# Performance work log

Measured on AMD Instinct MI355X. Metric: run time of the kernel, lower is better.

Reference implementation:

```python
import jax, jax.numpy as jnp
import numpy as np

# ---- hash-grid constants (from tcnn Encoding config in __init__) ----
N_LEVELS = 16
F = 2                      # n_features_per_level
LOG2_T = 19
T = 1 << LOG2_T            # hashmap entries per level
BASE_RES = 16
PER_LEVEL_SCALE = 1.447269237440378
PRIMES = np.array([1, 2654435761, 805459861], dtype=np.uint32)
# corner offsets of the unit cube, shape [8, 3]
OFFS = np.stack(np.meshgrid([0, 1], [0, 1], [0, 1], indexing='ij'), -1).reshape(8, 3)


def hash_grid_encode(x01, table):
    """x01: [N,3] in [0,1]; table: [L, T, F]. Returns [N, L*F]."""
    offs = jnp.asarray(OFFS, dtype=jnp.int32)          # [8,3]
    primes = jnp.asarray(PRIMES)                       # [3] uint32
    feats = []
    for l in range(N_LEVELS):
        scale = BASE_RES * (PER_LEVEL_SCALE ** l) - 1.0   # tcnn grid scale
        res = int(np.ceil(scale)) + 1                      # grid resolution
        pos = x01 * scale + 0.5                            # [N,3]
        pos0 = jnp.floor(pos)
        w = pos - pos0                                     # trilinear fracs [N,3]
        pos0 = pos0.astype(jnp.int32)
        corners = jnp.clip(pos0[:, None, :] + offs[None], 0, res - 1)  # [N,8,3]
        if res ** 3 <= T:
            # dense (stride) indexing fits in the table
            idx = (corners[..., 0]
                   + res * corners[..., 1]
                   + res * res * corners[..., 2]).astype(jnp.int32)    # [N,8]
        else:
            # spatial hash with uint32 wraparound multiply + xor
            cu = corners.astype(jnp.uint32)
            idx = ((cu[..., 0] * primes[0])
                   ^ (cu[..., 1] * primes[1])
                   ^ (cu[..., 2] * primes[2])) & jnp.uint32(T - 1)
            idx = idx.astype(jnp.int32)
        # trilinear weights: prod over dims of (w if offset==1 else 1-w)
        wc = jnp.where(offs[None].astype(bool), w[:, None, :], 1.0 - w[:, None, :])
        wc = wc.prod(-1)                                   # [N,8]
        g = table[l][idx]                                  # gather -> [N,8,F]
        feats.append(jnp.einsum('nc,ncf->nf', wc, g))      # [N,F]
    return jnp.concatenate(feats, -1)                      # [N, L*F]


def mlp2(x, w1, w2):
    # 2-layer bias-free MLP with ReLU, matching MLP(num_layers=2, bias=False)
    return jnp.maximum(x @ w1, 0.0) @ w2


def setup_inputs() -> dict:
    key = jax.random.key(0)
    ks = jax.random.split(key, 6)
    N = 1048576
    points = jax.random.uniform(ks[0], (N, 3), jnp.float32, -1.0, 1.0)  # in bbox [-1,1]^3
    # tcnn hash-grid init: uniform(-1e-4, 1e-4)
    hash_table = jax.random.uniform(ks[1], (N_LEVELS, T, F), jnp.float32, -1e-4, 1e-4)
    enc_dim = N_LEVELS * F  # 32
    dw1 = jax.random.normal(ks[2], (enc_dim, 64), jnp.float32) * (1.0 / np.sqrt(enc_dim))
    dw2 = jax.random.normal(ks[3], (64, 1), jnp.float32) * (1.0 / 8.0)
    fw1 = jax.random.normal(ks[4], (enc_dim, 64), jnp.float32) * (1.0 / np.sqrt(enc_dim))
    fw2 = jax.random.normal(ks[5], (64, 3), jnp.float32) * (1.0 / 8.0)
    return {"points": points, "hash_table": hash_table,
            "dw1": dw1, "dw2": dw2, "fw1": fw1, "fw2": fw2}


def reference(points, hash_table, dw1, dw2, fw1, fw2):
    # contract_to_unisphere with bbox [[-1,-1,-1],[1,1,1]] -> [0,1]^3, clamped
    x01 = jnp.clip((points + 1.0) * 0.5, 0.0, 1.0)
    enc = hash_grid_encode(x01, hash_table)               # [N, 32]
    density = jax.nn.softplus(mlp2(enc, dw1, dw2))        # [N, 1]
    color = jax.nn.sigmoid(mlp2(enc, fw1, fw2))           # [N, 3]
    return color, density
```

## Files before the change

### kernel.cpp

```cpp
#include <hip/hip_runtime.h>
#include <hip/hip_bf16.h>
#include <cmath>

#define NLV 16
#define TBL_SIZE (1u << 19)

struct LevelConsts {
    float scale[NLV];
    int   res[NLV];
    int   dense[NLV];
};

__device__ __forceinline__ unsigned int f32_to_bf16_rne(float f) {
    unsigned int u = __float_as_uint(f);
    return (u + 0x7FFFu + ((u >> 16) & 1u)) >> 16;
}
__device__ __forceinline__ unsigned int pack_bf16(float a, float b) {
    return f32_to_bf16_rne(a) | (f32_to_bf16_rne(b) << 16);
}
__device__ __forceinline__ short f32_to_bf16_s(float f) {
    return (short)f32_to_bf16_rne(f);
}
__device__ __forceinline__ float bf16lo_to_f32(unsigned int g) {
    return __uint_as_float(g << 16);
}
__device__ __forceinline__ float bf16hi_to_f32(unsigned int g) {
    return __uint_as_float(g & 0xFFFF0000u);
}

typedef __attribute__((ext_vector_type(8))) short bf16x8;
typedef __attribute__((ext_vector_type(4))) float f32x4;
typedef __attribute__((ext_vector_type(2))) unsigned int u32x2;
typedef __attribute__((ext_vector_type(4))) unsigned int u32x4;

__global__ __launch_bounds__(256) void cvt_table(const float* __restrict__ in,
                                                 unsigned int* __restrict__ out, int npairs) {
    int n2 = npairs >> 1;
    int i = blockIdx.x * 256 + threadIdx.x;
    int stride = gridDim.x * 256;
    const f32x4* in4 = (const f32x4*)in;
    u32x2* out2 = (u32x2*)out;
    for (; i < n2; i += stride) {
        f32x4 v = __builtin_nontemporal_load(&in4[i]);
        u32x2 o;
        o.x = pack_bf16(v.x, v.y);
        o.y = pack_bf16(v.z, v.w);
        __builtin_nontemporal_store(o, &out2[i]);
    }
}

#define ENC_P 4
__global__ __launch_bounds__(256) void encode_lvl(
    const float* __restrict__ points,
    const unsigned int* __restrict__ tbl,
    unsigned int* __restrict__ enc,
    int N, LevelConsts C)
{
    const int level = blockIdx.y;
    const float sc    = C.scale[level];
    const int   res   = C.res[level];
    const int   dense = C.dense[level];
    const unsigned int* __restrict__ t = tbl + (size_t)level * TBL_SIZE;
    unsigned int* __restrict__ eo = enc + (size_t)level * N;

    const int base = blockIdx.x * (256 * ENC_P) + threadIdx.x;

    int   pt[ENC_P];
    int   valid[ENC_P];
    float wx[ENC_P], wy[ENC_P], wz[ENC_P];
    unsigned int i0a[ENC_P][4], i1a[ENC_P][4];

#pragma unroll
    for (int q = 0; q < ENC_P; q++) {
        pt[q] = base + q * 256;
        valid[q] = pt[q] < N;
        int p = valid[q] ? pt[q] : 0;
        float px = __builtin_nontemporal_load(&points[p * 3 + 0]);
        float py = __builtin_nontemporal_load(&points[p * 3 + 1]);
        float pz = __builtin_nontemporal_load(&points[p * 3 + 2]);
        float x = fminf(fmaxf((px + 1.0f) * 0.5f, 0.0f), 1.0f);
        float y = fminf(fmaxf((py + 1.0f) * 0.5f, 0.0f), 1.0f);
        float z = fminf(fmaxf((pz + 1.0f) * 0.5f, 0.0f), 1.0f);

        float fx = x * sc + 0.5f;
        float fy = y * sc + 0.5f;
        float fz = z * sc + 0.5f;
        float f0x = floorf(fx), f0y = floorf(fy), f0z = floorf(fz);
        wx[q] = fx - f0x; wy[q] = fy - f0y; wz[q] = fz - f0z;
        int ix0 = min(max((int)f0x, 0), res - 1);
        int iy0 = min(max((int)f0y, 0), res - 1);
        int iz0 = min(max((int)f0z, 0), res - 1);
        int ix1 = min(ix0 + 1, res - 1);
        int iy1 = min(iy0 + 1, res - 1);
        int iz1 = min(iz0 + 1, res - 1);

#pragma unroll
        for (int m = 0; m < 4; m++) {
            unsigned int uy = (unsigned int)((m & 1) ? iy1 : iy0);
            unsigned int uz = (unsigned int)((m & 2) ? iz1 : iz0);
            unsigned int i0, i1;
            if (dense) {
                unsigned int b = (unsigned int)res * uy + (unsigned int)(res * res) * uz;
                i0 = (unsigned int)ix0 + b;
                i1 = (unsigned int)ix1 + b;
            } else {
                unsigned int H = uy * 2654435761u ^ uz * 805459861u;
                i0 = ((unsigned int)ix0 ^ H) & (TBL_SIZE - 1u);
                i1 = ((unsigned int)ix1 ^ H) & (TBL_SIZE - 1u);
            }
            i0a[q][m] = i0;
            i1a[q][m] = i1;
        }
    }

    u32x2       pr[ENC_P][4];
    unsigned int ex[ENC_P][4];
#pragma unroll
    for (int q = 0; q < ENC_P; q++) {
#pragma unroll
        for (int m = 0; m < 4; m++) {
            unsigned int i0 = i0a[q][m], i1 = i1a[q][m];
            pr[q][m] = *(const u32x2*)(t + (i0 & ~1u));
            unsigned int eidx = (i1 == (i0 ^ 1u)) ? i0 : i1;
            ex[q][m] = t[eidx];
        }
    }

#pragma unroll
    for (int q = 0; q < ENC_P; q++) {
        float e0 = 0.0f, e1 = 0.0f;
        float wxq = wx[q];
#pragma unroll
        for (int m = 0; m < 4; m++) {
            unsigned int i0 = i0a[q][m], i1 = i1a[q][m];
            u32x2 P = pr[q][m];
            unsigned int v0   = (i0 & 1u) ? P.y : P.x;
            unsigned int vpar = (i0 & 1u) ? P.x : P.y;
            unsigned int v1   = (i1 == (i0 ^ 1u)) ? vpar : ex[q][m];
            float wyz = (((m & 1) ? wy[q] : 1.0f - wy[q])) *
                        (((m & 2) ? wz[q] : 1.0f - wz[q]));
            float w0 = wyz * (1.0f - wxq);
            float w1 = wyz * wxq;
            e0 = fmaf(w0, bf16lo_to_f32(v0), e0);
            e0 = fmaf(w1, bf16lo_to_f32(v1), e0);
            e1 = fmaf(w0, bf16hi_to_f32(v0), e1);
            e1 = fmaf(w1, bf16hi_to_f32(v1), e1);
        }
        if (valid[q]) __builtin_nontemporal_store(pack_bf16(e0, e1), &eo[pt[q]]);
    }
}

__global__ __launch_bounds__(256, 4) void mlp_kernel(
    const unsigned int* __restrict__ enc,
    const float* __restrict__ dw1, const float* __restrict__ dw2,
    const float* __restrict__ fw1, const float* __restrict__ fw2,
    float* __restrict__ out, int N, int ntiles)
{
    __shared__ unsigned int hsh[4][16][68];
    __shared__ float sOut[4][256];

    const int tid  = threadIdx.x;
    const int wave = tid >> 6;
    const int lane = tid & 63;
    const int l15 = lane & 15;
    const int quad = lane >> 4;

    bf16x8 B1[8];
#pragma unroll
    for (int nt = 0; nt < 8; nt++) {
        int col = nt * 16 + l15;
        const float* w = (col < 64) ? (dw1 + col) : (fw1 + (col - 64));
#pragma unroll
        for (int j = 0; j < 8; j++) {
            int k = quad * 8 + j;
            B1[nt][j] = f32_to_bf16_s(w[k * 64]);
        }
    }

    bf16x8 B2[4];
#pragma unroll
    for (int s = 0; s < 4; s++) {
#pragma unroll
        for (int j = 0; j < 8; j++) {
            int k_lds = s * 32 + quad * 8 + j;
            int hu = ((k_lds & 7) << 4) | (k_lds >> 3);
            float v = 0.0f;
            if (l15 == 0)      v = (hu < 64)  ? dw2[hu] : 0.0f;
            else if (l15 < 4)  v = (hu >= 64) ? fw2[(hu - 64) * 3 + (l15 - 1)] : 0.0f;
            B2[s][j] = f32_to_bf16_s(v);
        }
    }

    for (int tile = blockIdx.x; tile < ntiles; tile += gridDim.x) {
        const int wbase = tile * 256 + wave * 64;

        unsigned int au[4][4];
#pragma unroll
        for (int sub = 0; sub < 4; sub++) {
            int ptc = min(wbase + sub * 16 + l15, N - 1);
#pragma unroll
            for (int j = 0; j < 4; j++)
                au[sub][j] = enc[(size_t)(quad * 4 + j) * N + ptc];
        }

#pragma unroll
        for (int sub = 0; sub < 4; sub++) {
            union { unsigned int u[4]; bf16x8 v; } acvt;
#pragma unroll
            for (int j = 0; j < 4; j++) acvt.u[j] = au[sub][j];

            f32x4 acc1[8];
#pragma unroll
            for (int nt = 0; nt < 8; nt++) {
                acc1[nt] = (f32x4){0.0f, 0.0f, 0.0f, 0.0f};
                acc1[nt] = __builtin_amdgcn_mfma_f32_16x16x32_bf16(acvt.v, B1[nt], acc1[nt], 0, 0, 0);
            }

#pragma unroll
            for (int r = 0; r < 4; r++) {
                u32x4 pk;
#pragma unroll
                for (int d = 0; d < 4; d++) {
                    float h0 = fmaxf(acc1[2 * d + 0][r], 0.0f);
                    float h1 = fmaxf(acc1[2 * d + 1][r], 0.0f);
                    pk[d] = pack_bf16(h0, h1);
                }
                *(u32x4*)&hsh[wave][quad * 4 + r][l15 * 4] = pk;
            }

            f32x4 p0 = (f32x4){0,0,0,0}, p1 = (f32x4){0,0,0,0};
            f32x4 p2 = (f32x4){0,0,0,0}, p3 = (f32x4){0,0,0,0};
            {
                bf16x8 a0 = *(const bf16x8*)&hsh[wave][l15][0 * 16 + quad * 4];
                bf16x8 a1 = *(const bf16x8*)&hsh[wave][l15][1 * 16 + quad * 4];
                bf16x8 a2 = *(const bf16x8*)&hsh[wave][l15][2 * 16 + quad * 4];
                bf16x8 a3 = *(const bf16x8*)&hsh[wave][l15][3 * 16 + quad * 4];
                p0 = __builtin_amdgcn_mfma_f32_16x16x32_bf16(a0, B2[0], p0, 0, 0, 0);
                p1 = __builtin_amdgcn_mfma_f32_16x16x32_bf16(a1, B2[1], p1, 0, 0, 0);
                p2 = __builtin_amdgcn_mfma_f32_16x16x32_bf16(a2, B2[2], p2, 0, 0, 0);
                p3 = __builtin_amdgcn_mfma_f32_16x16x32_bf16(a3, B2[3], p3, 0, 0, 0);
            }
            f32x4 acc2;
#pragma unroll
            for (int r = 0; r < 4; r++) acc2[r] = (p0[r] + p1[r]) + (p2[r] + p3[r]);

            if (l15 < 4) {
#pragma unroll
                for (int r = 0; r < 4; r++)
                    sOut[wave][(sub * 16 + quad * 4 + r) * 4 + l15] = acc2[r];
            }
        }

        long long cmax = ((long long)N - wbase) * 3;
#pragma unroll
        for (int round = 0; round < 3; round++) {
            int f = round * 64 + lane;
            int lp = f / 3, c = f - lp * 3;
            float v = sOut[wave][lp * 4 + 1 + c];
            v = 1.0f / (1.0f + expf(-v));
            if (f < cmax) out[(size_t)wbase * 3 + f] = v;
        }
        {
            int p = wbase + lane;
            float v = sOut[wave][lane * 4];
            v = (v > 20.0f) ? v : log1pf(expf(v));
            if (p < N) out[(size_t)3 * N + p] = v;
        }
    }
}

__global__ __launch_bounds__(256) void nerf_fused(
    const float* __restrict__ points,
    const float* __restrict__ table,
    const float* __restrict__ dw1, const float* __restrict__ dw2,
    const float* __restrict__ fw1, const float* __restrict__ fw2,
    float* __restrict__ out, int N, LevelConsts C)
{
    __shared__ float sD[64 * 32];
    __shared__ float sF[64 * 32];
    __shared__ float sDw2[64];
    __shared__ float sFw2[64 * 3];

    for (int idx = threadIdx.x; idx < 2048; idx += 256) {
        int i = idx >> 6;
        int j = idx & 63;
        sD[j * 32 + i] = dw1[idx];
        sF[j * 32 + i] = fw1[idx];
    }
    if (threadIdx.x < 64)  sDw2[threadIdx.x] = dw2[threadIdx.x];
    if (threadIdx.x < 192) sFw2[threadIdx.x] = fw2[threadIdx.x];
    __syncthreads();

    int gid = blockIdx.x * 256 + threadIdx.x;
    if (gid >= N) return;

    float px = points[gid * 3 + 0];
    float py = points[gid * 3 + 1];
    float pz = points[gid * 3 + 2];
    float x = fminf(fmaxf((px + 1.0f) * 0.5f, 0.0f), 1.0f);
    float y = fminf(fmaxf((py + 1.0f) * 0.5f, 0.0f), 1.0f);
    float z = fminf(fmaxf((pz + 1.0f) * 0.5f, 0.0f), 1.0f);

    float enc[32];

#pragma unroll
    for (int l = 0; l < NLV; l++) {
        const float sc = C.scale[l];
        const int   res = C.res[l];
        const int   dense = C.dense[l];
        const float* __restrict__ tbl = table + (size_t)l * TBL_SIZE * 2;

        float fx = x * sc + 0.5f;
        float fy = y * sc + 0.5f;
        float fz = z * sc + 0.5f;
        float f0x = floorf(fx), f0y = floorf(fy), f0z = floorf(fz);
        float wx = fx - f0x, wy = fy - f0y, wz = fz - f0z;
        int ix0 = min(max((int)f0x, 0), res - 1);
        int iy0 = min(max((int)f0y, 0), res - 1);
        int iz0 = min(max((int)f0z, 0), res - 1);
        int ix1 = min(ix0 + 1, res - 1);
        int iy1 = min(iy0 + 1, res - 1);
        int iz1 = min(iz0 + 1, res - 1);

        float e0 = 0.0f, e1 = 0.0f;
#pragma unroll
        for (int c = 0; c < 8; c++) {
            int cx = (c & 4) ? ix1 : ix0;
            int cy = (c & 2) ? iy1 : iy0;
            int cz = (c & 1) ? iz1 : iz0;
            float wgt = (((c & 4) ? wx : 1.0f - wx) *
                         ((c & 2) ? wy : 1.0f - wy)) *
                         ((c & 1) ? wz : 1.0f - wz);
            unsigned int idx;
            if (dense) {
                idx = (unsigned int)(cx + res * cy + res * res * cz);
            } else {
                idx = ((unsigned int)cx * 1u
                     ^ (unsigned int)cy * 2654435761u
                     ^ (unsigned int)cz * 805459861u) & (TBL_SIZE - 1u);
            }
            const float2 g = *(const float2*)(tbl + (size_t)idx * 2);
            e0 = fmaf(wgt, g.x, e0);
            e1 = fmaf(wgt, g.y, e1);
        }
        enc[2 * l + 0] = e0;
        enc[2 * l + 1] = e1;
    }

    float dacc = 0.0f, c0 = 0.0f, c1 = 0.0f, c2 = 0.0f;
    for (int j = 0; j < 64; j++) {
        float hd = 0.0f, hf = 0.0f;
        const float* __restrict__ colD = &sD[j * 32];
        const float* __restrict__ colF = &sF[j * 32];
#pragma unroll
        for (int i = 0; i < 32; i++) {
            hd = fmaf(enc[i], colD[i], hd);
            hf = fmaf(enc[i], colF[i], hf);
        }
        hd = fmaxf(hd, 0.0f);
        hf = fmaxf(hf, 0.0f);
        dacc = fmaf(hd, sDw2[j], dacc);
        c0 = fmaf(hf, sFw2[j * 3 + 0], c0);
        c1 = fmaf(hf, sFw2[j * 3 + 1], c1);
        c2 = fmaf(hf, sFw2[j * 3 + 2], c2);
    }

    float density = (dacc > 20.0f) ? dacc : log1pf(expf(dacc));
    out[gid * 3 + 0] = 1.0f / (1.0f + expf(-c0));
    out[gid * 3 + 1] = 1.0f / (1.0f + expf(-c1));
    out[gid * 3 + 2] = 1.0f / (1.0f + expf(-c2));
    out[(size_t)3 * N + gid] = density;
}

extern "C" void kernel_launch(void* const* d_in, const int* in_sizes, int n_in,
                              void* d_out, int out_size, void* d_ws, size_t ws_size,
                              hipStream_t stream) {
    const float* points = (const float*)d_in[0];
    const float* table  = (const float*)d_in[1];
    const float* dw1    = (const float*)d_in[2];
    const float* dw2    = (const float*)d_in[3];
    const float* fw1    = (const float*)d_in[4];
    const float* fw2    = (const float*)d_in[5];
    int N = in_sizes[0] / 3;

    LevelConsts C;
    for (int l = 0; l < NLV; l++) {
        double s = 16.0 * pow(1.447269237440378, (double)l) - 1.0;
        C.scale[l] = (float)s;
        int res = (int)ceil(s) + 1;
        C.res[l] = res;
        C.dense[l] = ((long long)res * res * res <= (long long)TBL_SIZE) ? 1 : 0;
    }

    const size_t tbl_bytes = (size_t)NLV * TBL_SIZE * 4;
    const size_t enc_bytes = (size_t)N * NLV * 4;
    if (ws_size >= tbl_bytes + enc_bytes) {
        unsigned int* tbl_bf16 = (unsigned int*)d_ws;
        unsigned int* enc_ws   = (unsigned int*)((char*)d_ws + tbl_bytes);

        int npairs = NLV * TBL_SIZE;
        cvt_table<<<1024, 256, 0, stream>>>(table, tbl_bf16, npairs);

        int chunks = (N + 256 * ENC_P - 1) / (256 * ENC_P);
        encode_lvl<<<dim3(chunks, NLV), 256, 0, stream>>>(points, tbl_bf16, enc_ws, N, C);

        int ntiles = (N + 255) / 256;
        mlp_kernel<<<1792, 256, 0, stream>>>(enc_ws, dw1, dw2, fw1, fw2,
                                             (float*)d_out, N, ntiles);
    } else {
        int blocks = (N + 255) / 256;
        nerf_fused<<<blocks, 256, 0, stream>>>(points, table, dw1, dw2, fw1, fw2,
                                               (float*)d_out, N, C);
    }
}
```

Baseline: 535.1 us.

## Sort points by Morton bucket before hash-grid encoding for gather locality

```diff
diff --git a/kernel.cpp b/kernel.cpp
--- a/kernel.cpp
+++ b/kernel.cpp
@@ -4,6 +4,7 @@
 
 #define NLV 16
 #define TBL_SIZE (1u << 19)
+#define NB (1 << 18)
 
 struct LevelConsts {
     float scale[NLV];
@@ -46,6 +47,109 @@
         o.x = pack_bf16(v.x, v.y);
         o.y = pack_bf16(v.z, v.w);
         __builtin_nontemporal_store(o, &out2[i]);
+    }
+}
+
+__device__ __forceinline__ unsigned spread3(unsigned x) {
+    x &= 0x3FFu;
+    x = (x | (x << 16)) & 0x030000FFu;
+    x = (x | (x << 8))  & 0x0300F00Fu;
+    x = (x | (x << 4))  & 0x030C30C3u;
+    x = (x | (x << 2))  & 0x09249249u;
+    return x;
+}
+__device__ __forceinline__ unsigned bucket_key(float px, float py, float pz) {
+    float x = fminf(fmaxf((px + 1.0f) * 0.5f, 0.0f), 1.0f);
+    float y = fminf(fmaxf((py + 1.0f) * 0.5f, 0.0f), 1.0f);
+    float z = fminf(fmaxf((pz + 1.0f) * 0.5f, 0.0f), 1.0f);
+    int ix = min((int)(x * 64.0f), 63);
+    int iy = min((int)(y * 64.0f), 63);
+    int iz = min((int)(z * 64.0f), 63);
+    return spread3((unsigned)ix) | (spread3((unsigned)iy) << 1) | (spread3((unsigned)iz) << 2);
+}
+
+__global__ __launch_bounds__(256) void zero_u32(unsigned* __restrict__ p, int n) {
+    int i = blockIdx.x * 256 + threadIdx.x;
+    if (i < n) p[i] = 0u;
+}
+
+__global__ __launch_bounds__(256) void bucket_hist(const float* __restrict__ pts,
+                                                   unsigned* __restrict__ hist, int N) {
+    int i = blockIdx.x * 256 + threadIdx.x;
+    int stride = gridDim.x * 256;
+    for (; i < N; i += stride) {
+        float px = pts[3 * i + 0];
+        float py = pts[3 * i + 1];
+        float pz = pts[3 * i + 2];
+        atomicAdd(&hist[bucket_key(px, py, pz)], 1u);
+    }
+}
+
+__device__ __forceinline__ unsigned block_excl_scan_256(unsigned v, unsigned* wtot) {
+    int t = threadIdx.x;
+    int lane = t & 63, wid = t >> 6;
+    unsigned x = v;
+#pragma unroll
+    for (int d = 1; d < 64; d <<= 1) {
+        unsigned y = __shfl_up(x, d, 64);
+        if (lane >= d) x += y;
+    }
+    unsigned wex = x - v;
+    if (lane == 63) wtot[wid] = x;
+    __syncthreads();
+    if (t == 0) {
+        unsigned r = 0;
+        for (int i = 0; i < 4; i++) { unsigned tt = wtot[i]; wtot[i] = r; r += tt; }
+    }
+    __syncthreads();
+    return wex + wtot[wid];
+}
+
+__global__ __launch_bounds__(256) void scan1(const unsigned* __restrict__ hist,
+                                             unsigned* __restrict__ base,
+                                             unsigned* __restrict__ bsum) {
+    __shared__ unsigned wtot[4];
+    int t = threadIdx.x, b = blockIdx.x;
+    unsigned v = hist[b * 256 + t];
+    unsigned ex = block_excl_scan_256(v, wtot);
+    base[b * 256 + t] = ex;
+    if (t == 255) bsum[b] = ex + v;
+}
+
+__global__ __launch_bounds__(256) void scan2(unsigned* __restrict__ bsum) {
+    __shared__ unsigned wtot[4];
+    int t = threadIdx.x;
+    unsigned s[4];
+    unsigned tot = 0;
+#pragma unroll
+    for (int j = 0; j < 4; j++) { s[j] = bsum[4 * t + j]; tot += s[j]; }
+    unsigned ex = block_excl_scan_256(tot, wtot);
+    unsigned run = ex;
+#pragma unroll
+    for (int j = 0; j < 4; j++) { unsigned sv = s[j]; bsum[4 * t + j] = run; run += sv; }
+}
+
+__global__ __launch_bounds__(256) void scan3(unsigned* __restrict__ base,
+                                             const unsigned* __restrict__ bsum) {
+    base[blockIdx.x * 256 + threadIdx.x] += bsum[blockIdx.x];
+}
+
+__global__ __launch_bounds__(256) void bucket_scatter(const float* __restrict__ pts,
+                                                      unsigned* __restrict__ base,
+                                                      float* __restrict__ spts,
+                                                      unsigned* __restrict__ perm, int N) {
+    int i = blockIdx.x * 256 + threadIdx.x;
+    int stride = gridDim.x * 256;
+    for (; i < N; i += stride) {
+        float px = pts[3 * i + 0];
+        float py = pts[3 * i + 1];
+        float pz = pts[3 * i + 2];
+        unsigned k = bucket_key(px, py, pz);
+        unsigned pos = atomicAdd(&base[k], 1u);
+        spts[3 * pos + 0] = px;
+        spts[3 * pos + 1] = py;
+        spts[3 * pos + 2] = pz;
+        perm[pos] = (unsigned)i;
     }
 }
 
@@ -154,6 +258,7 @@
     const unsigned int* __restrict__ enc,
     const float* __restrict__ dw1, const float* __restrict__ dw2,
     const float* __restrict__ fw1, const float* __restrict__ fw2,
+    const unsigned int* __restrict__ perm,
     float* __restrict__ out, int N, int ntiles)
 {
     __shared__ unsigned int hsh[4][16][68];
@@ -251,20 +356,37 @@
             }
         }
 
-        long long cmax = ((long long)N - wbase) * 3;
-#pragma unroll
-        for (int round = 0; round < 3; round++) {
-            int f = round * 64 + lane;
-            int lp = f / 3, c = f - lp * 3;
-            float v = sOut[wave][lp * 4 + 1 + c];
-            v = 1.0f / (1.0f + expf(-v));
-            if (f < cmax) out[(size_t)wbase * 3 + f] = v;
-        }
-        {
+        if (perm) {
             int p = wbase + lane;
-            float v = sOut[wave][lane * 4];
-            v = (v > 20.0f) ? v : log1pf(expf(v));
-            if (p < N) out[(size_t)3 * N + p] = v;
+            if (p < N) {
+                unsigned int o = perm[p];
+                f32x4 v = *(const f32x4*)&sOut[wave][lane * 4];
+                float d = v[0];
+                d = (d > 20.0f) ? d : log1pf(expf(d));
+                out[(size_t)3 * N + o] = d;
+                float r0 = 1.0f / (1.0f + expf(-v[1]));
+                float g0 = 1.0f / (1.0f + expf(-v[2]));
+                float b0 = 1.0f / (1.0f + expf(-v[3]));
+                out[(size_t)o * 3 + 0] = r0;
+                out[(size_t)o * 3 + 1] = g0;
+                out[(size_t)o * 3 + 2] = b0;
+            }
+        } else {
+            long long cmax = ((long long)N - wbase) * 3;
+#pragma unroll
+            for (int round = 0; round < 3; round++) {
+                int f = round * 64 + lane;
+                int lp = f / 3, c = f - lp * 3;
+                float v = sOut[wave][lp * 4 + 1 + c];
+                v = 1.0f / (1.0f + expf(-v));
+                if (f < cmax) out[(size_t)wbase * 3 + f] = v;
+            }
+            {
+                int p = wbase + lane;
+                float v = sOut[wave][lane * 4];
+                v = (v > 20.0f) ? v : log1pf(expf(v));
+                if (p < N) out[(size_t)3 * N + p] = v;
+            }
         }
     }
 }
@@ -392,9 +514,45 @@
         C.dense[l] = ((long long)res * res * res <= (long long)TBL_SIZE) ? 1 : 0;
     }
 
-    const size_t tbl_bytes = (size_t)NLV * TBL_SIZE * 4;
-    const size_t enc_bytes = (size_t)N * NLV * 4;
-    if (ws_size >= tbl_bytes + enc_bytes) {
+    auto align256 = [](size_t x) { return (x + 255) & ~(size_t)255; };
+    const size_t tbl_bytes  = align256((size_t)NLV * TBL_SIZE * 4);
+    const size_t enc_bytes  = align256((size_t)N * NLV * 4);
+    const size_t spts_bytes = align256((size_t)N * 3 * 4);
+    const size_t perm_bytes = align256((size_t)N * 4);
+    const size_t hist_bytes = align256((size_t)NB * 4);
+    const size_t base_bytes = align256((size_t)NB * 4);
+    const size_t bsum_bytes = align256((size_t)(NB / 256) * 4);
+    const size_t sort_total = tbl_bytes + enc_bytes + spts_bytes + perm_bytes
+                            + hist_bytes + base_bytes + bsum_bytes;
+
+    if (ws_size >= sort_total) {
+        char* wp = (char*)d_ws;
+        unsigned int* tbl_bf16 = (unsigned int*)wp;            wp += tbl_bytes;
+        unsigned int* enc_ws   = (unsigned int*)wp;            wp += enc_bytes;
+        float*        spts     = (float*)wp;                   wp += spts_bytes;
+        unsigned int* perm     = (unsigned int*)wp;            wp += perm_bytes;
+        unsigned int* hist     = (unsigned int*)wp;            wp += hist_bytes;
+        unsigned int* base     = (unsigned int*)wp;            wp += base_bytes;
+        unsigned int* bsum     = (unsigned int*)wp;            wp += bsum_bytes;
+
+        int npairs = NLV * TBL_SIZE;
+        cvt_table<<<1024, 256, 0, stream>>>(table, tbl_bf16, npairs);
+
+        int pblocks = min((N + 255) / 256, 2048);
+        zero_u32<<<NB / 256, 256, 0, stream>>>(hist, NB);
+        bucket_hist<<<pblocks, 256, 0, stream>>>(points, hist, N);
+        scan1<<<NB / 256, 256, 0, stream>>>(hist, base, bsum);
+        scan2<<<1, 256, 0, stream>>>(bsum);
+        scan3<<<NB / 256, 256, 0, stream>>>(base, bsum);
+        bucket_scatter<<<pblocks, 256, 0, stream>>>(points, base, spts, perm, N);
+
+        int chunks = (N + 256 * ENC_P - 1) / (256 * ENC_P);
+        encode_lvl<<<dim3(chunks, NLV), 256, 0, stream>>>(spts, tbl_bf16, enc_ws, N, C);
+
+        int ntiles = (N + 255) / 256;
+        mlp_kernel<<<1792, 256, 0, stream>>>(enc_ws, dw1, dw2, fw1, fw2, perm,
+                                             (float*)d_out, N, ntiles);
+    } else if (ws_size >= tbl_bytes + enc_bytes) {
         unsigned int* tbl_bf16 = (unsigned int*)d_ws;
         unsigned int* enc_ws   = (unsigned int*)((char*)d_ws + tbl_bytes);
 
@@ -405,7 +563,7 @@
         encode_lvl<<<dim3(chunks, NLV), 256, 0, stream>>>(points, tbl_bf16, enc_ws, N, C);
 
         int ntiles = (N + 255) / 256;
-        mlp_kernel<<<1792, 256, 0, stream>>>(enc_ws, dw1, dw2, fw1, fw2,
+        mlp_kernel<<<1792, 256, 0, stream>>>(enc_ws, dw1, dw2, fw1, fw2, nullptr,
                                              (float*)d_out, N, ntiles);
     } else {
         int blocks = (N + 255) / 256;
```

Result: slower. 563.7 us (+5.3%).
